# Performance work log

Measured on AMD Instinct MI355X. Metric: run time of the kernel, lower is better.

The kernel has to match this reference:

```python
import jax, jax.numpy as jnp
import numpy as np

D_MODEL, D_STATE, EXPAND = 1024, 256, 2
BATCH, SEQ = 8, 2048


def setup_inputs() -> dict:
    key = jax.random.key(0)
    ks = jax.random.split(key, 7)
    s = 0.02
    return {
        "x": jax.random.normal(ks[0], (BATCH, SEQ, D_MODEL), jnp.float32),
        "W_in": jax.random.normal(ks[1], (D_MODEL, D_MODEL * EXPAND), jnp.float32) * s,
        "b_in": jax.random.normal(ks[2], (D_MODEL * EXPAND,), jnp.float32) * s,
        "W_state": jax.random.normal(ks[3], (D_MODEL * EXPAND, D_STATE), jnp.float32) * s,
        "b_state": jax.random.normal(ks[4], (D_STATE,), jnp.float32) * s,
        "W_out": jax.random.normal(ks[5], (D_STATE, D_MODEL), jnp.float32) * s,
        "b_out": jax.random.normal(ks[6], (D_MODEL,), jnp.float32) * s,
        "init_state": jnp.zeros((1, D_STATE), jnp.float32),
    }


def reference(x, W_in, b_in, W_state, b_state, W_out, b_out, init_state):
    # x: [B, T, D]
    x_proj = jax.nn.silu(jnp.einsum("btd,de->bte", x, W_in) + b_in)  # [B,T,2D]
    # state_proj depends only on x_proj, so batch the GEMM over all timesteps
    updates = jnp.einsum("bte,es->bts", x_proj, W_state) + b_state    # [B,T,S]
    updates_t = jnp.swapaxes(updates, 0, 1)                            # [T,B,S]
    state0 = jnp.broadcast_to(init_state, (x.shape[0], init_state.shape[1]))

    def step(state, u):
        new = jax.nn.silu(state + u)
        return new, new

    _, states = jax.lax.scan(step, state0, updates_t)  # [T,B,S]
    out = jnp.einsum("tbs,sd->tbd", states, W_out) + b_out  # [T,B,D]
    return jnp.swapaxes(out, 0, 1)  # [B,T,D]
```

## Files before the change

kernel.cpp:

```cpp
#include <hip/hip_runtime.h>
#include <cstdint>
#include <cstddef>

#define BATCH 8
#define SEQ   2048
#define DM    1024
#define DE    2048
#define DSZ   256
#define MROWS (BATCH*SEQ)

typedef __bf16 bf16;
typedef __bf16 bf16x8 __attribute__((ext_vector_type(8)));
typedef _Float16 f16;
typedef _Float16 f16x8 __attribute__((ext_vector_type(8)));
typedef float  f32x4  __attribute__((ext_vector_type(4)));

__device__ __forceinline__ void glds16(const void* gp, void* lp) {
  __builtin_amdgcn_global_load_lds(
      (const __attribute__((address_space(1))) void*)gp,
      (__attribute__((address_space(3))) void*)lp, 16, 0, 0);
}

__device__ __forceinline__ float silu_f(float x) {
  return x * __builtin_amdgcn_rcpf(1.0f + __expf(-x));
}

__global__ void transpose_split_k(const float* __restrict__ in, f16* __restrict__ oh,
                                  f16* __restrict__ ol, int R, int C) {
  __shared__ float tile[32][33];
  const int c0 = blockIdx.x * 32, r0 = blockIdx.y * 32;
  const int tx = threadIdx.x, ty = threadIdx.y;
  #pragma unroll
  for (int i = 0; i < 4; ++i)
    tile[ty + i*8][tx] = in[(size_t)(r0 + ty + i*8) * C + c0 + tx];
  __syncthreads();
  #pragma unroll
  for (int i = 0; i < 4; ++i) {
    float v = tile[tx][ty + i*8];
    f16 h = (f16)v;
    size_t idx = (size_t)(c0 + ty + i*8) * R + r0 + tx;
    oh[idx] = h;
    ol[idx] = (f16)(v - (float)h);
  }
}

__global__ void transpose_cast_k(const float* __restrict__ in, bf16* __restrict__ out, int R, int C) {
  __shared__ float tile[32][33];
  const int c0 = blockIdx.x * 32, r0 = blockIdx.y * 32;
  const int tx = threadIdx.x, ty = threadIdx.y;
  #pragma unroll
  for (int i = 0; i < 4; ++i)
    tile[ty + i*8][tx] = in[(size_t)(r0 + ty + i*8) * C + c0 + tx];
  __syncthreads();
  #pragma unroll
  for (int i = 0; i < 4; ++i)
    out[(size_t)(c0 + ty + i*8) * R + r0 + tx] = (bf16)tile[tx][ty + i*8];
}

__global__ __launch_bounds__(256) void gemm1_k(const float* __restrict__ A,
                                               const f16* __restrict__ Bth,
                                               const f16* __restrict__ Btl,
                                               const float* __restrict__ bias,
                                               f16* __restrict__ Ch, f16* __restrict__ Cl) {
  const int K = 1024, N = 2048;
  extern __shared__ char smraw[];
  float* sA  = (float*)smraw;
  f16*   sBh = (f16*)(smraw + 16384);
  f16*   sBl = (f16*)(smraw + 24576);

  const int tid = threadIdx.x;
  const int w = tid >> 6, l = tid & 63;
  const int bm = blockIdx.y * 128, bn = blockIdx.x * 128;
  const int wm = (w >> 1) * 64, wn = (w & 1) * 64;
  const int lr = l & 15, lq = l >> 4;

  const float* pA[4]; float* dA[4];
  #pragma unroll
  for (int p = 0; p < 4; ++p) {
    const int c = p * 256 + tid;
    const int kq = c >> 8, m = (c >> 1) & 127, half = c & 1;
    pA[p] = A + (size_t)(bm + m) * K + kq * 8 + half * 4;
    dA[p] = sA + (size_t)c * 4;
  }
  const f16* pBh[2]; const f16* pBl[2]; f16* dBh[2]; f16* dBl[2];
  #pragma unroll
  for (int p = 0; p < 2; ++p) {
    const int c = p * 256 + tid;
    const int n = c >> 2, k8 = c & 3;
    pBh[p] = Bth + (size_t)(bn + n) * K + k8 * 8;
    pBl[p] = Btl + (size_t)(bn + n) * K + k8 * 8;
    dBh[p] = sBh + (size_t)c * 8;
    dBl[p] = sBl + (size_t)c * 8;
  }

  int offA[4], offB[4];
  #pragma unroll
  for (int i = 0; i < 4; ++i) {
    offA[i] = lq * 1024 + (wm + i*16 + lr) * 8;
    offB[i] = (wn + i*16 + lr) * 32 + lq * 8;
  }

  f32x4 acc[4][4] = {};

  for (int kk = 0; kk < K; kk += 32) {
    __syncthreads();
    #pragma unroll
    for (int p = 0; p < 4; ++p) { glds16(pA[p], dA[p]); pA[p] += 32; }
    #pragma unroll
    for (int p = 0; p < 2; ++p) {
      glds16(pBh[p], dBh[p]); pBh[p] += 32;
      glds16(pBl[p], dBl[p]); pBl[p] += 32;
    }
    asm volatile("s_waitcnt vmcnt(0)" ::: "memory");
    __syncthreads();

    f16x8 ahf[4], alf[4], bhf[4], blf[4];
    #pragma unroll
    for (int i = 0; i < 4; ++i) {
      f32x4 a0 = *(const f32x4*)(sA + offA[i]);
      f32x4 a1 = *(const f32x4*)(sA + offA[i] + 4);
      #pragma unroll
      for (int j = 0; j < 4; ++j) {
        float v0 = a0[j], v1 = a1[j];
        f16 h0 = (f16)v0, h1 = (f16)v1;
        ahf[i][j]   = h0; alf[i][j]   = (f16)(v0 - (float)h0);
        ahf[i][4+j] = h1; alf[i][4+j] = (f16)(v1 - (float)h1);
      }
    }
    #pragma unroll
    for (int j = 0; j < 4; ++j) {
      bhf[j] = *(const f16x8*)(sBh + offB[j]);
      blf[j] = *(const f16x8*)(sBl + offB[j]);
    }
    #pragma unroll
    for (int i = 0; i < 4; ++i)
      #pragma unroll
      for (int j = 0; j < 4; ++j) {
        acc[i][j] = __builtin_amdgcn_mfma_f32_16x16x32_f16(ahf[i], bhf[j], acc[i][j], 0, 0, 0);
        acc[i][j] = __builtin_amdgcn_mfma_f32_16x16x32_f16(ahf[i], blf[j], acc[i][j], 0, 0, 0);
        acc[i][j] = __builtin_amdgcn_mfma_f32_16x16x32_f16(alf[i], bhf[j], acc[i][j], 0, 0, 0);
      }
  }

  #pragma unroll
  for (int j = 0; j < 4; ++j) {
    const int col = bn + wn + j*16 + lr;
    const float bv = bias[col];
    #pragma unroll
    for (int i = 0; i < 4; ++i)
      #pragma unroll
      for (int r = 0; r < 4; ++r) {
        const int row = bm + wm + i*16 + lq*4 + r;
        const float s = silu_f(acc[i][j][r] + bv);
        const f16 h = (f16)s;
        const size_t idx = (size_t)row * N + col;
        Ch[idx] = h;
        Cl[idx] = (f16)(s - (float)h);
      }
  }
}

__global__ __launch_bounds__(256) void gemm2_k(const f16* __restrict__ Ah, const f16* __restrict__ Al,
                                               const f16* __restrict__ Bh, const f16* __restrict__ Bl,
                                               const float* __restrict__ bias,
                                               float* __restrict__ C, int N, int K) {
  extern __shared__ char smraw[];
  f16* sAh = (f16*)smraw;
  f16* sAl = (f16*)(smraw + 8192);
  f16* sBh = (f16*)(smraw + 16384);
  f16* sBl = (f16*)(smraw + 24576);

  const int tid = threadIdx.x;
  const int w = tid >> 6, l = tid & 63;
  const int bm = blockIdx.y * 128, bn = blockIdx.x * 128;
  const int wm = (w >> 1) * 64, wn = (w & 1) * 64;
  const int lr = l & 15, lq = l >> 4;

  const f16 *pAh[2], *pAl[2], *pBh[2], *pBl[2];
  f16 *dAh[2], *dAl[2], *dBh[2], *dBl[2];
  #pragma unroll
  for (int p = 0; p < 2; ++p) {
    const int c = p * 256 + tid;
    const int r = c >> 2, k8 = c & 3;
    pAh[p] = Ah + (size_t)(bm + r) * K + k8 * 8;
    pAl[p] = Al + (size_t)(bm + r) * K + k8 * 8;
    pBh[p] = Bh + (size_t)(bn + r) * K + k8 * 8;
    pBl[p] = Bl + (size_t)(bn + r) * K + k8 * 8;
    dAh[p] = sAh + (size_t)c * 8; dAl[p] = sAl + (size_t)c * 8;
    dBh[p] = sBh + (size_t)c * 8; dBl[p] = sBl + (size_t)c * 8;
  }

  int offA[4], offB[4];
  #pragma unroll
  for (int i = 0; i < 4; ++i) {
    offA[i] = (wm + i*16 + lr) * 32 + lq * 8;
    offB[i] = (wn + i*16 + lr) * 32 + lq * 8;
  }

  f32x4 acc[4][4] = {};

  for (int kk = 0; kk < K; kk += 32) {
    __syncthreads();
    #pragma unroll
    for (int p = 0; p < 2; ++p) {
      glds16(pAh[p], dAh[p]); pAh[p] += 32;
      glds16(pAl[p], dAl[p]); pAl[p] += 32;
      glds16(pBh[p], dBh[p]); pBh[p] += 32;
      glds16(pBl[p], dBl[p]); pBl[p] += 32;
    }
    asm volatile("s_waitcnt vmcnt(0)" ::: "memory");
    __syncthreads();

    f16x8 ahf[4], alf[4], bhf[4], blf[4];
    #pragma unroll
    for (int i = 0; i < 4; ++i) {
      ahf[i] = *(const f16x8*)(sAh + offA[i]);
      alf[i] = *(const f16x8*)(sAl + offA[i]);
    }
    #pragma unroll
    for (int j = 0; j < 4; ++j) {
      bhf[j] = *(const f16x8*)(sBh + offB[j]);
      blf[j] = *(const f16x8*)(sBl + offB[j]);
    }
    #pragma unroll
    for (int i = 0; i < 4; ++i)
      #pragma unroll
      for (int j = 0; j < 4; ++j) {
        acc[i][j] = __builtin_amdgcn_mfma_f32_16x16x32_f16(ahf[i], bhf[j], acc[i][j], 0, 0, 0);
        acc[i][j] = __builtin_amdgcn_mfma_f32_16x16x32_f16(ahf[i], blf[j], acc[i][j], 0, 0, 0);
        acc[i][j] = __builtin_amdgcn_mfma_f32_16x16x32_f16(alf[i], bhf[j], acc[i][j], 0, 0, 0);
      }
  }

  #pragma unroll
  for (int j = 0; j < 4; ++j) {
    const int col = bn + wn + j*16 + lr;
    const float bv = bias[col];
    #pragma unroll
    for (int i = 0; i < 4; ++i)
      #pragma unroll
      for (int r = 0; r < 4; ++r) {
        const int row = bm + wm + i*16 + lq*4 + r;
        C[(size_t)row * N + col] = acc[i][j][r] + bv;
      }
  }
}

__global__ __launch_bounds__(256) void gemm3_k(const bf16* __restrict__ A,
                                               const bf16* __restrict__ Bt,
                                               const float* __restrict__ bias,
                                               float* __restrict__ C, int N, int K) {
  extern __shared__ char smraw[];
  bf16* sA = (bf16*)smraw;
  bf16* sB = (bf16*)(smraw + 8192);

  const int tid = threadIdx.x;
  const int w = tid >> 6, l = tid & 63;
  const int bm = blockIdx.y * 128, bn = blockIdx.x * 128;
  const int wm = (w >> 1) * 64, wn = (w & 1) * 64;
  const int lr = l & 15, lq = l >> 4;

  const bf16* pA[2]; const bf16* pB[2];
  bf16* ldsA[2]; bf16* ldsB[2];
  #pragma unroll
  for (int p = 0; p < 2; ++p) {
    const int c = (p*4 + w)*64 + l;
    pA[p] = A  + (size_t)(bm + (c >> 2)) * K + (c & 3) * 8;
    pB[p] = Bt + (size_t)(bn + (c >> 2)) * K + (c & 3) * 8;
    ldsA[p] = sA + (size_t)c * 8;
    ldsB[p] = sB + (size_t)c * 8;
  }

  int offA[4], offB[4];
  #pragma unroll
  for (int i = 0; i < 4; ++i) {
    offA[i] = (wm + i*16 + lr) * 32 + lq * 8;
    offB[i] = (wn + i*16 + lr) * 32 + lq * 8;
  }

  f32x4 acc[4][4] = {};

  for (int kk = 0; kk < K; kk += 32) {
    __syncthreads();
    glds16(pA[0], ldsA[0]); glds16(pA[1], ldsA[1]);
    glds16(pB[0], ldsB[0]); glds16(pB[1], ldsB[1]);
    pA[0] += 32; pA[1] += 32; pB[0] += 32; pB[1] += 32;
    asm volatile("s_waitcnt vmcnt(0)" ::: "memory");
    __syncthreads();

    bf16x8 af[4], bfr[4];
    #pragma unroll
    for (int i = 0; i < 4; ++i) af[i]  = *(const bf16x8*)(sA + offA[i]);
    #pragma unroll
    for (int j = 0; j < 4; ++j) bfr[j] = *(const bf16x8*)(sB + offB[j]);
    #pragma unroll
    for (int i = 0; i < 4; ++i)
      #pragma unroll
      for (int j = 0; j < 4; ++j)
        acc[i][j] = __builtin_amdgcn_mfma_f32_16x16x32_bf16(af[i], bfr[j], acc[i][j], 0, 0, 0);
  }

  #pragma unroll
  for (int j = 0; j < 4; ++j) {
    const int col = bn + wn + j*16 + lr;
    const float bv = bias[col];
    #pragma unroll
    for (int i = 0; i < 4; ++i)
      #pragma unroll
      for (int r = 0; r < 4; ++r) {
        const int row = bm + wm + i*16 + lq*4 + r;
        C[(size_t)row * N + col] = acc[i][j][r] + bv;
      }
  }
}

__global__ void scan_k(const float* __restrict__ upd, const float* __restrict__ init,
                       bf16* __restrict__ states) {
  const int b = blockIdx.x, s = threadIdx.x;
  const float* u = upd + (size_t)b * SEQ * DSZ + s;
  bf16* st = states + (size_t)b * SEQ * DSZ + s;
  float state = init[s];
  float ubuf[16];
  #pragma unroll
  for (int i = 0; i < 16; ++i) ubuf[i] = u[(size_t)i * DSZ];
  for (int t0 = 0; t0 < SEQ; t0 += 16) {
    #pragma unroll
    for (int i = 0; i < 16; ++i) {
      const int t = t0 + i;
      const float x = state + ubuf[i];
      state = silu_f(x);
      st[(size_t)t * DSZ] = (bf16)state;
      const int tn = t + 16;
      ubuf[i] = (tn < SEQ) ? u[(size_t)tn * DSZ] : 0.0f;
    }
  }
}

extern "C" void kernel_launch(void* const* d_in, const int* in_sizes, int n_in,
                              void* d_out, int out_size, void* d_ws, size_t ws_size,
                              hipStream_t stream) {
  const float* x       = (const float*)d_in[0];
  const float* W_in    = (const float*)d_in[1];
  const float* b_in    = (const float*)d_in[2];
  const float* W_state = (const float*)d_in[3];
  const float* b_state = (const float*)d_in[4];
  const float* W_out   = (const float*)d_in[5];
  const float* b_out   = (const float*)d_in[6];
  const float* init_st = (const float*)d_in[7];
  float* out = (float*)d_out;

  char* ws = (char*)d_ws;
  float* upd        = (float*)(ws + 0);
  bf16*  states_b   = (bf16*)(ws + 16777216);
  f16*   w_in_t_h   = (f16*)(ws + 25165824);
  f16*   w_in_t_l   = (f16*)(ws + 29360128);
  f16*   w_state_t_h= (f16*)(ws + 33554432);
  f16*   w_state_t_l= (f16*)(ws + 34603008);
  bf16*  w_out_t    = (bf16*)(ws + 35651584);
  f16*   xproj_h    = (f16*)(ws + 36175872);
  f16*   xproj_l    = (f16*)(ws + 103284736);

  dim3 tb(32, 8);
  transpose_split_k<<<dim3(DE/32,  DM/32), tb, 0, stream>>>(W_in,    w_in_t_h,    w_in_t_l,    DM,  DE);
  transpose_split_k<<<dim3(DSZ/32, DE/32), tb, 0, stream>>>(W_state, w_state_t_h, w_state_t_l, DE,  DSZ);
  transpose_cast_k <<<dim3(DM/32,  DSZ/32), tb, 0, stream>>>(W_out,  w_out_t,     DSZ, DM);

  gemm1_k<<<dim3(DE/128, MROWS/128), 256, 32768, stream>>>(x, w_in_t_h, w_in_t_l, b_in, xproj_h, xproj_l);

  gemm2_k<<<dim3(DSZ/128, MROWS/128), 256, 32768, stream>>>(xproj_h, xproj_l, w_state_t_h, w_state_t_l,
                                                            b_state, upd, DSZ, DE);

  scan_k<<<BATCH, DSZ, 0, stream>>>(upd, init_st, states_b);

  gemm3_k<<<dim3(DM/128, MROWS/128), 256, 16384, stream>>>(states_b, w_out_t, b_out, out, DM, DSZ);
}
```

Measured before the change: 613.7 us.

## Pre-split x to f16 pairs, chunk GEMM1/GEMM2 over rows, retile GEMMs

Adds a separate pass that splits x into high/low f16 halves, so GEMM1 no longer converts fp32 A tiles inside its inner loop. GEMM1 now runs 512 threads with a 4x2 warp grid, and GEMM2 uses smaller 64-row tiles to launch more blocks. GEMM1 and GEMM2 run in two row chunks that reuse one x_proj buffer, which keeps the intermediate in cache. GEMM3 and the states buffer switch from bf16 to f16. The cost is an extra full read and write of x for the split, and serialised chunk launches.

```diff
diff --git a/kernel.cpp b/kernel.cpp
--- a/kernel.cpp
+++ b/kernel.cpp
@@ -8,10 +8,10 @@
 #define DE    2048
 #define DSZ   256
 #define MROWS (BATCH*SEQ)
-
-typedef __bf16 bf16;
-typedef __bf16 bf16x8 __attribute__((ext_vector_type(8)));
+#define MCHUNK 8192
+
 typedef _Float16 f16;
+typedef _Float16 f16x4 __attribute__((ext_vector_type(4)));
 typedef _Float16 f16x8 __attribute__((ext_vector_type(8)));
 typedef float  f32x4  __attribute__((ext_vector_type(4)));
 
@@ -23,6 +23,22 @@
 
 __device__ __forceinline__ float silu_f(float x) {
   return x * __builtin_amdgcn_rcpf(1.0f + __expf(-x));
+}
+
+__global__ void split_x_k(const float* __restrict__ in, f16* __restrict__ oh,
+                          f16* __restrict__ ol, int n) {
+  int i = (blockIdx.x * blockDim.x + threadIdx.x) * 4;
+  const int stride = gridDim.x * blockDim.x * 4;
+  for (; i < n; i += stride) {
+    float4 v = *(const float4*)(in + i);
+    f16x4 h, l;
+    h[0] = (f16)v.x; l[0] = (f16)(v.x - (float)h[0]);
+    h[1] = (f16)v.y; l[1] = (f16)(v.y - (float)h[1]);
+    h[2] = (f16)v.z; l[2] = (f16)(v.z - (float)h[2]);
+    h[3] = (f16)v.w; l[3] = (f16)(v.w - (float)h[3]);
+    *(f16x4*)(oh + i) = h;
+    *(f16x4*)(ol + i) = l;
+  }
 }
 
 __global__ void transpose_split_k(const float* __restrict__ in, f16* __restrict__ oh,
@@ -44,7 +60,7 @@
   }
 }
 
-__global__ void transpose_cast_k(const float* __restrict__ in, bf16* __restrict__ out, int R, int C) {
+__global__ void transpose_cast_f16_k(const float* __restrict__ in, f16* __restrict__ out, int R, int C) {
   __shared__ float tile[32][33];
   const int c0 = blockIdx.x * 32, r0 = blockIdx.y * 32;
   const int tx = threadIdx.x, ty = threadIdx.y;
@@ -54,19 +70,173 @@
   __syncthreads();
   #pragma unroll
   for (int i = 0; i < 4; ++i)
-    out[(size_t)(c0 + ty + i*8) * R + r0 + tx] = (bf16)tile[tx][ty + i*8];
-}
-
-__global__ __launch_bounds__(256) void gemm1_k(const float* __restrict__ A,
-                                               const f16* __restrict__ Bth,
-                                               const f16* __restrict__ Btl,
+    out[(size_t)(c0 + ty + i*8) * R + r0 + tx] = (f16)tile[tx][ty + i*8];
+}
+
+__global__ __launch_bounds__(512) void gemm1_k(const f16* __restrict__ Ah, const f16* __restrict__ Al,
+                                               const f16* __restrict__ Bh, const f16* __restrict__ Bl,
                                                const float* __restrict__ bias,
                                                f16* __restrict__ Ch, f16* __restrict__ Cl) {
   const int K = 1024, N = 2048;
-  extern __shared__ char smraw[];
-  float* sA  = (float*)smraw;
-  f16*   sBh = (f16*)(smraw + 16384);
-  f16*   sBl = (f16*)(smraw + 24576);
+  __shared__ f16 sAh[4096], sAl[4096], sBh[4096], sBl[4096];
+
+  const int tid = threadIdx.x;
+  const int w = tid >> 6, l = tid & 63;
+  const int bm = blockIdx.y * 128, bn = blockIdx.x * 128;
+  const int wm = (w >> 2) * 64, wn = (w & 3) * 32;
+  const int lr = l & 15, lq = l >> 4;
+
+  const int r = tid >> 2, k8 = tid & 3;
+  const f16* pAh = Ah + (size_t)(bm + r) * K + k8 * 8;
+  const f16* pAl = Al + (size_t)(bm + r) * K + k8 * 8;
+  const f16* pBh = Bh + (size_t)(bn + r) * K + k8 * 8;
+  const f16* pBl = Bl + (size_t)(bn + r) * K + k8 * 8;
+  f16* dAh = sAh + tid * 8; f16* dAl = sAl + tid * 8;
+  f16* dBh = sBh + tid * 8; f16* dBl = sBl + tid * 8;
+
+  int offA[4], offB[2];
+  #pragma unroll
+  for (int i = 0; i < 4; ++i) offA[i] = (wm + i*16 + lr) * 32 + lq * 8;
+  #pragma unroll
+  for (int j = 0; j < 2; ++j) offB[j] = (wn + j*16 + lr) * 32 + lq * 8;
+
+  f32x4 acc[4][2] = {};
+
+  for (int kk = 0; kk < K; kk += 32) {
+    __syncthreads();
+    glds16(pAh, dAh); glds16(pAl, dAl);
+    glds16(pBh, dBh); glds16(pBl, dBl);
+    pAh += 32; pAl += 32; pBh += 32; pBl += 32;
+    asm volatile("s_waitcnt vmcnt(0)" ::: "memory");
+    __syncthreads();
+
+    f16x8 ah[4], al[4], bh[2], bl[2];
+    #pragma unroll
+    for (int i = 0; i < 4; ++i) {
+      ah[i] = *(const f16x8*)(sAh + offA[i]);
+      al[i] = *(const f16x8*)(sAl + offA[i]);
+    }
+    #pragma unroll
+    for (int j = 0; j < 2; ++j) {
+      bh[j] = *(const f16x8*)(sBh + offB[j]);
+      bl[j] = *(const f16x8*)(sBl + offB[j]);
+    }
+    #pragma unroll
+    for (int i = 0; i < 4; ++i)
+      #pragma unroll
+      for (int j = 0; j < 2; ++j) {
+        acc[i][j] = __builtin_amdgcn_mfma_f32_16x16x32_f16(ah[i], bh[j], acc[i][j], 0, 0, 0);
+        acc[i][j] = __builtin_amdgcn_mfma_f32_16x16x32_f16(ah[i], bl[j], acc[i][j], 0, 0, 0);
+        acc[i][j] = __builtin_amdgcn_mfma_f32_16x16x32_f16(al[i], bh[j], acc[i][j], 0, 0, 0);
+      }
+  }
+
+  #pragma unroll
+  for (int j = 0; j < 2; ++j) {
+    const int col = bn + wn + j*16 + lr;
+    const float bv = bias[col];
+    #pragma unroll
+    for (int i = 0; i < 4; ++i)
+      #pragma unroll
+      for (int r4 = 0; r4 < 4; ++r4) {
+        const int row = bm + wm + i*16 + lq*4 + r4;
+        const float s = silu_f(acc[i][j][r4] + bv);
+        const f16 h = (f16)s;
+        const size_t idx = (size_t)row * N + col;
+        Ch[idx] = h;
+        Cl[idx] = (f16)(s - (float)h);
+      }
+  }
+}
+
+__global__ __launch_bounds__(256) void gemm2s_k(const f16* __restrict__ Ah, const f16* __restrict__ Al,
+                                                const f16* __restrict__ Bh, const f16* __restrict__ Bl,
+                                                const float* __restrict__ bias,
+                                                float* __restrict__ C) {
+  const int K = 2048, N = 256;
+  __shared__ f16 sAh[2048], sAl[2048], sBh[4096], sBl[4096];
+
+  const int tid = threadIdx.x;
+  const int w = tid >> 6, l = tid & 63;
+  const int bm = blockIdx.y * 64, bn = blockIdx.x * 128;
+  const int wm = (w & 1) * 32, wn = (w >> 1) * 64;
+  const int lr = l & 15, lq = l >> 4;
+
+  const int rA = tid >> 2, k8 = tid & 3;
+  const f16* pAh = Ah + (size_t)(bm + rA) * K + k8 * 8;
+  const f16* pAl = Al + (size_t)(bm + rA) * K + k8 * 8;
+  f16* dAh = sAh + tid * 8; f16* dAl = sAl + tid * 8;
+  const f16 *pBh[2], *pBl[2]; f16 *dBh[2], *dBl[2];
+  #pragma unroll
+  for (int p = 0; p < 2; ++p) {
+    const int c = p * 256 + tid;
+    const int rB = c >> 2;
+    pBh[p] = Bh + (size_t)(bn + rB) * K + (c & 3) * 8;
+    pBl[p] = Bl + (size_t)(bn + rB) * K + (c & 3) * 8;
+    dBh[p] = sBh + (size_t)c * 8; dBl[p] = sBl + (size_t)c * 8;
+  }
+
+  int offA[2], offB[4];
+  #pragma unroll
+  for (int i = 0; i < 2; ++i) offA[i] = (wm + i*16 + lr) * 32 + lq * 8;
+  #pragma unroll
+  for (int j = 0; j < 4; ++j) offB[j] = (wn + j*16 + lr) * 32 + lq * 8;
+
+  f32x4 acc[2][4] = {};
+
+  for (int kk = 0; kk < K; kk += 32) {
+    __syncthreads();
+    glds16(pAh, dAh); glds16(pAl, dAl);
+    pAh += 32; pAl += 32;
+    #pragma unroll
+    for (int p = 0; p < 2; ++p) {
+      glds16(pBh[p], dBh[p]); pBh[p] += 32;
+      glds16(pBl[p], dBl[p]); pBl[p] += 32;
+    }
+    asm volatile("s_waitcnt vmcnt(0)" ::: "memory");
+    __syncthreads();
+
+    f16x8 ah[2], al[2], bh[4], bl[4];
+    #pragma unroll
+    for (int i = 0; i < 2; ++i) {
+      ah[i] = *(const f16x8*)(sAh + offA[i]);
+      al[i] = *(const f16x8*)(sAl + offA[i]);
+    }
+    #pragma unroll
+    for (int j = 0; j < 4; ++j) {
+      bh[j] = *(const f16x8*)(sBh + offB[j]);
+      bl[j] = *(const f16x8*)(sBl + offB[j]);
+    }
+    #pragma unroll
+    for (int i = 0; i < 2; ++i)
+      #pragma unroll
+      for (int j = 0; j < 4; ++j) {
+        acc[i][j] = __builtin_amdgcn_mfma_f32_16x16x32_f16(ah[i], bh[j], acc[i][j], 0, 0, 0);
+        acc[i][j] = __builtin_amdgcn_mfma_f32_16x16x32_f16(ah[i], bl[j], acc[i][j], 0, 0, 0);
+        acc[i][j] = __builtin_amdgcn_mfma_f32_16x16x32_f16(al[i], bh[j], acc[i][j], 0, 0, 0);
+      }
+  }
+
+  #pragma unroll
+  for (int j = 0; j < 4; ++j) {
+    const int col = bn + wn + j*16 + lr;
+    const float bv = bias[col];
+    #pragma unroll
+    for (int i = 0; i < 2; ++i)
+      #pragma unroll
+      for (int r4 = 0; r4 < 4; ++r4) {
+        const int row = bm + wm + i*16 + lq*4 + r4;
+        C[(size_t)row * N + col] = acc[i][j][r4] + bv;
+      }
+  }
+}
+
+__global__ __launch_bounds__(256) void gemm3_k(const f16* __restrict__ A,
+                                               const f16* __restrict__ Bt,
+                                               const float* __restrict__ bias,
+                                               float* __restrict__ C) {
+  const int K = 256, N = 1024;
+  __shared__ f16 sA[4096], sB[4096];
 
   const int tid = threadIdx.x;
   const int w = tid >> 6, l = tid & 63;
@@ -74,29 +244,21 @@
   const int wm = (w >> 1) * 64, wn = (w & 1) * 64;
   const int lr = l & 15, lq = l >> 4;
 
-  const float* pA[4]; float* dA[4];
-  #pragma unroll
-  for (int p = 0; p < 4; ++p) {
-    const int c = p * 256 + tid;
-    const int kq = c >> 8, m = (c >> 1) & 127, half = c & 1;
-    pA[p] = A + (size_t)(bm + m) * K + kq * 8 + half * 4;
-    dA[p] = sA + (size_t)c * 4;
-  }
-  const f16* pBh[2]; const f16* pBl[2]; f16* dBh[2]; f16* dBl[2];
+  const f16 *pA[2], *pB[2]; f16 *dA[2], *dB[2];
   #pragma unroll
   for (int p = 0; p < 2; ++p) {
     const int c = p * 256 + tid;
-    const int n = c >> 2, k8 = c & 3;
-    pBh[p] = Bth + (size_t)(bn + n) * K + k8 * 8;
-    pBl[p] = Btl + (size_t)(bn + n) * K + k8 * 8;
-    dBh[p] = sBh + (size_t)c * 8;
-    dBl[p] = sBl + (size_t)c * 8;
+    const int r = c >> 2, k8 = c & 3;
+    pA[p] = A  + (size_t)(bm + r) * K + k8 * 8;
+    pB[p] = Bt + (size_t)(bn + r) * K + k8 * 8;
+    dA[p] = sA + (size_t)c * 8;
+    dB[p] = sB + (size_t)c * 8;
   }
 
   int offA[4], offB[4];
   #pragma unroll
   for (int i = 0; i < 4; ++i) {
-    offA[i] = lq * 1024 + (wm + i*16 + lr) * 8;
+    offA[i] = (wm + i*16 + lr) * 32 + lq * 8;
     offB[i] = (wn + i*16 + lr) * 32 + lq * 8;
   }
 
@@ -104,42 +266,22 @@
 
   for (int kk = 0; kk < K; kk += 32) {
     __syncthreads();
-    #pragma unroll
-    for (int p = 0; p < 4; ++p) { glds16(pA[p], dA[p]); pA[p] += 32; }
-    #pragma unroll
-    for (int p = 0; p < 2; ++p) {
-      glds16(pBh[p], dBh[p]); pBh[p] += 32;
-      glds16(pBl[p], dBl[p]); pBl[p] += 32;
-    }
+    glds16(pA[0], dA[0]); glds16(pA[1], dA[1]);
+    glds16(pB[0], dB[0]); glds16(pB[1], dB[1]);
+    pA[0] += 32; pA[1] += 32; pB[0] += 32; pB[1] += 32;
     asm volatile("s_waitcnt vmcnt(0)" ::: "memory");
     __syncthreads();
 
-    f16x8 ahf[4], alf[4], bhf[4], blf[4];
-    #pragma unroll
-    for (int i = 0; i < 4; ++i) {
-      f32x4 a0 = *(const f32x4*)(sA + offA[i]);
-      f32x4 a1 = *(const f32x4*)(sA + offA[i] + 4);
-      #pragma unroll
-      for (int j = 0; j < 4; ++j) {
-        float v0 = a0[j], v1 = a1[j];
-        f16 h0 = (f16)v0, h1 = (f16)v1;
-        ahf[i][j]   = h0; alf[i][j]   = (f16)(v0 - (float)h0);
-        ahf[i][4+j] = h1; alf[i][4+j] = (f16)(v1 - (float)h1);
-      }
-    }
-    #pragma unroll
-    for (int j = 0; j < 4; ++j) {
-      bhf[j] = *(const f16x8*)(sBh + offB[j]);
-      blf[j] = *(const f16x8*)(sBl + offB[j]);
-    }
+    f16x8 af[4], bfr[4];
+    #pragma unroll
+    for (int i = 0; i < 4; ++i) af[i]  = *(const f16x8*)(sA + offA[i]);
+    #pragma unroll
+    for (int j = 0; j < 4; ++j) bfr[j] = *(const f16x8*)(sB + offB[j]);
     #pragma unroll
     for (int i = 0; i < 4; ++i)
       #pragma unroll
-      for (int j = 0; j < 4; ++j) {
-        acc[i][j] = __builtin_amdgcn_mfma_f32_16x16x32_f16(ahf[i], bhf[j], acc[i][j], 0, 0, 0);
-        acc[i][j] = __builtin_amdgcn_mfma_f32_16x16x32_f16(ahf[i], blf[j], acc[i][j], 0, 0, 0);
-        acc[i][j] = __builtin_amdgcn_mfma_f32_16x16x32_f16(alf[i], bhf[j], acc[i][j], 0, 0, 0);
-      }
+      for (int j = 0; j < 4; ++j)
+        acc[i][j] = __builtin_amdgcn_mfma_f32_16x16x32_f16(af[i], bfr[j], acc[i][j], 0, 0, 0);
   }
 
   #pragma unroll
@@ -149,176 +291,18 @@
     #pragma unroll
     for (int i = 0; i < 4; ++i)
       #pragma unroll
-      for (int r = 0; r < 4; ++r) {
-        const int row = bm + wm + i*16 + lq*4 + r;
-        const float s = silu_f(acc[i][j][r] + bv);
-        const f16 h = (f16)s;
-        const size_t idx = (size_t)row * N + col;
-        Ch[idx] = h;
-        Cl[idx] = (f16)(s - (float)h);
-      }
-  }
-}
-
-__global__ __launch_bounds__(256) void gemm2_k(const f16* __restrict__ Ah, const f16* __restrict__ Al,
-                                               const f16* __restrict__ Bh, const f16* __restrict__ Bl,
-                                               const float* __restrict__ bias,
-                                               float* __restrict__ C, int N, int K) {
-  extern __shared__ char smraw[];
-  f16* sAh = (f16*)smraw;
-  f16* sAl = (f16*)(smraw + 8192);
-  f16* sBh = (f16*)(smraw + 16384);
-  f16* sBl = (f16*)(smraw + 24576);
-
-  const int tid = threadIdx.x;
-  const int w = tid >> 6, l = tid & 63;
-  const int bm = blockIdx.y * 128, bn = blockIdx.x * 128;
-  const int wm = (w >> 1) * 64, wn = (w & 1) * 64;
-  const int lr = l & 15, lq = l >> 4;
-
-  const f16 *pAh[2], *pAl[2], *pBh[2], *pBl[2];
-  f16 *dAh[2], *dAl[2], *dBh[2], *dBl[2];
-  #pragma unroll
-  for (int p = 0; p < 2; ++p) {
-    const int c = p * 256 + tid;
-    const int r = c >> 2, k8 = c & 3;
-    pAh[p] = Ah + (size_t)(bm + r) * K + k8 * 8;
-    pAl[p] = Al + (size_t)(bm + r) * K + k8 * 8;
-    pBh[p] = Bh + (size_t)(bn + r) * K + k8 * 8;
-    pBl[p] = Bl + (size_t)(bn + r) * K + k8 * 8;
-    dAh[p] = sAh + (size_t)c * 8; dAl[p] = sAl + (size_t)c * 8;
-    dBh[p] = sBh + (size_t)c * 8; dBl[p] = sBl + (size_t)c * 8;
-  }
-
-  int offA[4], offB[4];
-  #pragma unroll
-  for (int i = 0; i < 4; ++i) {
-    offA[i] = (wm + i*16 + lr) * 32 + lq * 8;
-    offB[i] = (wn + i*16 + lr) * 32 + lq * 8;
-  }
-
-  f32x4 acc[4][4] = {};
-
-  for (int kk = 0; kk < K; kk += 32) {
-    __syncthreads();
-    #pragma unroll
-    for (int p = 0; p < 2; ++p) {
-      glds16(pAh[p], dAh[p]); pAh[p] += 32;
-      glds16(pAl[p], dAl[p]); pAl[p] += 32;
-      glds16(pBh[p], dBh[p]); pBh[p] += 32;
-      glds16(pBl[p], dBl[p]); pBl[p] += 32;
-    }
-    asm volatile("s_waitcnt vmcnt(0)" ::: "memory");
-    __syncthreads();
-
-    f16x8 ahf[4], alf[4], bhf[4], blf[4];
-    #pragma unroll
-    for (int i = 0; i < 4; ++i) {
-      ahf[i] = *(const f16x8*)(sAh + offA[i]);
-      alf[i] = *(const f16x8*)(sAl + offA[i]);
-    }
-    #pragma unroll
-    for (int j = 0; j < 4; ++j) {
-      bhf[j] = *(const f16x8*)(sBh + offB[j]);
-      blf[j] = *(const f16x8*)(sBl + offB[j]);
-    }
-    #pragma unroll
-    for (int i = 0; i < 4; ++i)
-      #pragma unroll
-      for (int j = 0; j < 4; ++j) {
-        acc[i][j] = __builtin_amdgcn_mfma_f32_16x16x32_f16(ahf[i], bhf[j], acc[i][j], 0, 0, 0);
-        acc[i][j] = __builtin_amdgcn_mfma_f32_16x16x32_f16(ahf[i], blf[j], acc[i][j], 0, 0, 0);
-        acc[i][j] = __builtin_amdgcn_mfma_f32_16x16x32_f16(alf[i], bhf[j], acc[i][j], 0, 0, 0);
-      }
-  }
-
-  #pragma unroll
-  for (int j = 0; j < 4; ++j) {
-    const int col = bn + wn + j*16 + lr;
-    const float bv = bias[col];
-    #pragma unroll
-    for (int i = 0; i < 4; ++i)
-      #pragma unroll
-      for (int r = 0; r < 4; ++r) {
-        const int row = bm + wm + i*16 + lq*4 + r;
-        C[(size_t)row * N + col] = acc[i][j][r] + bv;
-      }
-  }
-}
-
-__global__ __launch_bounds__(256) void gemm3_k(const bf16* __restrict__ A,
-                                               const bf16* __restrict__ Bt,
-                                               const float* __restrict__ bias,
-                                               float* __restrict__ C, int N, int K) {
-  extern __shared__ char smraw[];
-  bf16* sA = (bf16*)smraw;
-  bf16* sB = (bf16*)(smraw + 8192);
-
-  const int tid = threadIdx.x;
-  const int w = tid >> 6, l = tid & 63;
-  const int bm = blockIdx.y * 128, bn = blockIdx.x * 128;
-  const int wm = (w >> 1) * 64, wn = (w & 1) * 64;
-  const int lr = l & 15, lq = l >> 4;
-
-  const bf16* pA[2]; const bf16* pB[2];
-  bf16* ldsA[2]; bf16* ldsB[2];
-  #pragma unroll
-  for (int p = 0; p < 2; ++p) {
-    const int c = (p*4 + w)*64 + l;
-    pA[p] = A  + (size_t)(bm + (c >> 2)) * K + (c & 3) * 8;
-    pB[p] = Bt + (size_t)(bn + (c >> 2)) * K + (c & 3) * 8;
-    ldsA[p] = sA + (size_t)c * 8;
-    ldsB[p] = sB + (size_t)c * 8;
-  }
-
-  int offA[4], offB[4];
-  #pragma unroll
-  for (int i = 0; i < 4; ++i) {
-    offA[i] = (wm + i*16 + lr) * 32 + lq * 8;
-    offB[i] = (wn + i*16 + lr) * 32 + lq * 8;
-  }
-
-  f32x4 acc[4][4] = {};
-
-  for (int kk = 0; kk < K; kk += 32) {
-    __syncthreads();
-    glds16(pA[0], ldsA[0]); glds16(pA[1], ldsA[1]);
-    glds16(pB[0], ldsB[0]); glds16(pB[1], ldsB[1]);
-    pA[0] += 32; pA[1] += 32; pB[0] += 32; pB[1] += 32;
-    asm volatile("s_waitcnt vmcnt(0)" ::: "memory");
-    __syncthreads();
-
-    bf16x8 af[4], bfr[4];
-    #pragma unroll
-    for (int i = 0; i < 4; ++i) af[i]  = *(const bf16x8*)(sA + offA[i]);
-    #pragma unroll
-    for (int j = 0; j < 4; ++j) bfr[j] = *(const bf16x8*)(sB + offB[j]);
-    #pragma unroll
-    for (int i = 0; i < 4; ++i)
-      #pragma unroll
-      for (int j = 0; j < 4; ++j)
-        acc[i][j] = __builtin_amdgcn_mfma_f32_16x16x32_bf16(af[i], bfr[j], acc[i][j], 0, 0, 0);
-  }
-
-  #pragma unroll
-  for (int j = 0; j < 4; ++j) {
-    const int col = bn + wn + j*16 + lr;
-    const float bv = bias[col];
-    #pragma unroll
-    for (int i = 0; i < 4; ++i)
-      #pragma unroll
-      for (int r = 0; r < 4; ++r) {
-        const int row = bm + wm + i*16 + lq*4 + r;
-        C[(size_t)row * N + col] = acc[i][j][r] + bv;
+      for (int r4 = 0; r4 < 4; ++r4) {
+        const int row = bm + wm + i*16 + lq*4 + r4;
+        C[(size_t)row * N + col] = acc[i][j][r4] + bv;
       }
   }
 }
 
 __global__ void scan_k(const float* __restrict__ upd, const float* __restrict__ init,
-                       bf16* __restrict__ states) {
+                       f16* __restrict__ states) {
   const int b = blockIdx.x, s = threadIdx.x;
   const float* u = upd + (size_t)b * SEQ * DSZ + s;
-  bf16* st = states + (size_t)b * SEQ * DSZ + s;
+  f16* st = states + (size_t)b * SEQ * DSZ + s;
   float state = init[s];
   float ubuf[16];
   #pragma unroll
@@ -329,7 +313,7 @@
       const int t = t0 + i;
       const float x = state + ubuf[i];
       state = silu_f(x);
-      st[(size_t)t * DSZ] = (bf16)state;
+      st[(size_t)t * DSZ] = (f16)state;
       const int tn = t + 16;
       ubuf[i] = (tn < SEQ) ? u[(size_t)tn * DSZ] : 0.0f;
     }
@@ -350,27 +334,33 @@
   float* out = (float*)d_out;
 
   char* ws = (char*)d_ws;
-  float* upd        = (float*)(ws + 0);
-  bf16*  states_b   = (bf16*)(ws + 16777216);
-  f16*   w_in_t_h   = (f16*)(ws + 25165824);
-  f16*   w_in_t_l   = (f16*)(ws + 29360128);
-  f16*   w_state_t_h= (f16*)(ws + 33554432);
-  f16*   w_state_t_l= (f16*)(ws + 34603008);
-  bf16*  w_out_t    = (bf16*)(ws + 35651584);
-  f16*   xproj_h    = (f16*)(ws + 36175872);
-  f16*   xproj_l    = (f16*)(ws + 103284736);
-
+  f16*   xh        = (f16*)(ws + 0);
+  f16*   xl        = (f16*)(ws + 33554432);
+  f16*   xproj_h   = (f16*)(ws + 67108864);
+  f16*   xproj_l   = (f16*)(ws + 100663296);
+  float* upd       = (float*)(ws + 134217728);
+  f16*   states    = (f16*)(ws + 150994944);
+  f16*   w_in_h    = (f16*)(ws + 159383552);
+  f16*   w_in_l    = (f16*)(ws + 163577856);
+  f16*   w_state_h = (f16*)(ws + 167772160);
+  f16*   w_state_l = (f16*)(ws + 168820736);
+  f16*   w_out_t   = (f16*)(ws + 169869312);
+
+  split_x_k<<<4096, 256, 0, stream>>>(x, xh, xl, MROWS * DM);
   dim3 tb(32, 8);
-  transpose_split_k<<<dim3(DE/32,  DM/32), tb, 0, stream>>>(W_in,    w_in_t_h,    w_in_t_l,    DM,  DE);
-  transpose_split_k<<<dim3(DSZ/32, DE/32), tb, 0, stream>>>(W_state, w_state_t_h, w_state_t_l, DE,  DSZ);
-  transpose_cast_k <<<dim3(DM/32,  DSZ/32), tb, 0, stream>>>(W_out,  w_out_t,     DSZ, DM);
-
-  gemm1_k<<<dim3(DE/128, MROWS/128), 256, 32768, stream>>>(x, w_in_t_h, w_in_t_l, b_in, xproj_h, xproj_l);
-
-  gemm2_k<<<dim3(DSZ/128, MROWS/128), 256, 32768, stream>>>(xproj_h, xproj_l, w_state_t_h, w_state_t_l,
-                                                            b_state, upd, DSZ, DE);
-
-  scan_k<<<BATCH, DSZ, 0, stream>>>(upd, init_st, states_b);
-
-  gemm3_k<<<dim3(DM/128, MROWS/128), 256, 16384, stream>>>(states_b, w_out_t, b_out, out, DM, DSZ);
-}
+  transpose_split_k<<<dim3(DE/32,  DM/32), tb, 0, stream>>>(W_in,    w_in_h,    w_in_l,    DM,  DE);
+  transpose_split_k<<<dim3(DSZ/32, DE/32), tb, 0, stream>>>(W_state, w_state_h, w_state_l, DE,  DSZ);
+  transpose_cast_f16_k<<<dim3(DM/32, DSZ/32), tb, 0, stream>>>(W_out, w_out_t, DSZ, DM);
+
+  for (int c = 0; c < 2; ++c) {
+    const size_t ro = (size_t)c * MCHUNK;
+    gemm1_k<<<dim3(DE/128, MCHUNK/128), 512, 0, stream>>>(
+        xh + ro * DM, xl + ro * DM, w_in_h, w_in_l, b_in, xproj_h, xproj_l);
+    gemm2s_k<<<dim3(DSZ/128, MCHUNK/64), 256, 0, stream>>>(
+        xproj_h, xproj_l, w_state_h, w_state_l, b_state, upd + ro * DSZ);
+  }
+
+  scan_k<<<BATCH, DSZ, 0, stream>>>(upd, init_st, states);
+
+  gemm3_k<<<dim3(DM/128, MROWS/128), 256, 0, stream>>>(states, w_out_t, b_out, out);
+}
```

Result: slower. 633.2 us (+3.2%).
